# Performance work log

Measured on AMD Instinct MI355X. Metric: run time of the kernel, lower is better.

The kernel has to match this reference:

```python
import jax, jax.numpy as jnp
import numpy as np

B, T, M, E = 2, 2048, 1024, 8
CAP = (2 * B * T) // E  # GShard top-2 capacity = 2*S/E = 1024


def setup_inputs() -> dict:
    key = jax.random.key(0)
    k1, k2, k3 = jax.random.split(key, 3)
    x = jax.random.normal(k1, (B, T, M), jnp.float32)
    wg = jax.random.normal(k2, (M, E), jnp.float32) * 0.02
    expert_w = jax.random.normal(k3, (E, M, M), jnp.float32) * 0.02
    expert_b = jnp.zeros((E, M), jnp.float32)
    return {"x": x, "wg": wg, "expert_w": expert_w, "expert_b": expert_b}


def _top2_gate(x2, wg, capacity):
    """fairseq/GShard Top2Gate (deterministic second-expert, no jitter).
    Returns (l_aux, combine_weights[S,E,C], dispatch_mask[S,E,C] bool)."""
    S = x2.shape[0]
    num_experts = wg.shape[1]
    logits = x2 @ wg                                  # [S, E]
    gates = jax.nn.softmax(logits, axis=-1)           # [S, E]
    # top-1 expert
    idx1 = jnp.argmax(gates, axis=1)
    mask1 = jax.nn.one_hot(idx1, num_experts, dtype=jnp.int32)
    # top-2 expert: argmax over logits with top-1 masked out
    neg_inf = jnp.finfo(logits.dtype).min
    logits_wo1 = jnp.where(mask1.astype(bool), neg_inf, logits)
    idx2 = jnp.argmax(logits_wo1, axis=1)
    mask2 = jax.nn.one_hot(idx2, num_experts, dtype=jnp.int32)
    # positions within each expert's buffer
    loc1 = jnp.cumsum(mask1, axis=0) - 1              # [S, E]
    loc2 = jnp.cumsum(mask2, axis=0) - 1 + jnp.sum(mask1, axis=0, keepdims=True)
    # load-balancing auxiliary loss
    me = jnp.mean(gates, axis=0)
    ce = jnp.mean(mask1.astype(gates.dtype), axis=0)
    l_aux = jnp.mean(me * ce) * (num_experts * num_experts)
    # drop tokens over capacity
    mask1 = mask1 * (loc1 < capacity).astype(jnp.int32)
    mask2 = mask2 * (loc2 < capacity).astype(jnp.int32)
    loc1_s = jnp.sum(loc1 * mask1, axis=1)            # [S]
    loc2_s = jnp.sum(loc2 * mask2, axis=1)
    m1f = mask1.astype(gates.dtype)
    m2f = mask2.astype(gates.dtype)
    gates1_s = jnp.sum(gates * m1f, axis=1)
    gates2_s = jnp.sum(gates * m2f, axis=1)
    denom = gates1_s + gates2_s
    denom = jnp.clip(denom, jnp.finfo(gates.dtype).eps, None)
    gates1 = gates1_s / denom
    gates2 = gates2_s / denom
    loc1_oh = jax.nn.one_hot(loc1_s, capacity, dtype=gates.dtype)  # [S, C]
    loc2_oh = jax.nn.one_hot(loc2_s, capacity, dtype=gates.dtype)
    combine1 = gates1[:, None, None] * m1f[:, :, None] * loc1_oh[:, None, :]
    combine2 = gates2[:, None, None] * m2f[:, :, None] * loc2_oh[:, None, :]
    combine_weights = combine1 + combine2             # [S, E, C]
    dispatch_mask = combine_weights > 0               # bool [S, E, C]
    return l_aux, combine_weights, dispatch_mask


def reference(x, wg, expert_w, expert_b):
    b, t, d = x.shape
    x2 = x.reshape(-1, d)                             # [S, M]
    l_aux, cw, dm = _top2_gate(x2, wg, CAP)
    dmf = dm.astype(x.dtype)                          # [S, E, C]
    # dispatch: (E*C, S) @ (S, M) -> per-expert token buffers [E, C, M]
    dispatched = jnp.einsum('sec,sm->ecm', dmf, x2)
    # per-expert Linear (single device: all experts local, all-to-all = identity)
    expert_out = jnp.einsum('ecm,emn->ecn', dispatched, expert_w) + expert_b[:, None, :]
    # combine: (S, E*C) @ (E*C, M) -> [S, M]
    combined = jnp.einsum('sec,ecm->sm', cw, expert_out)
    return combined.reshape(b, t, d), l_aux
```

## Files before the change

kernel.cpp:

```cpp
#include <hip/hip_runtime.h>

typedef unsigned short u16;
typedef unsigned int u32;
typedef unsigned long long u64;
typedef short v8s __attribute__((ext_vector_type(8)));
typedef float v4f __attribute__((ext_vector_type(4)));

#define S_TOK 4096
#define MDIM  1024
#define NEXP  8
#define CAPN  1024

__device__ __forceinline__ u16 f2bf(float f) {
  u32 u = __float_as_uint(f);
  u += 0x7FFFu + ((u >> 16) & 1u);
  return (u16)(u >> 16);
}
__device__ __forceinline__ float bf2f(u16 h) {
  return __uint_as_float(((u32)h) << 16);
}
__device__ __forceinline__ void gll16(const void* g, void* l) {
  __builtin_amdgcn_global_load_lds(
      (const __attribute__((address_space(1))) void*)g,
      (__attribute__((address_space(3))) void*)l, 16, 0, 0);
}

__global__ __launch_bounds__(256) void prep_kernel(const float* __restrict__ x,
                                                   const float* __restrict__ wg,
                                                   const float* __restrict__ w,
                                                   u16* __restrict__ xbf,
                                                   u16* __restrict__ wT,
                                                   int4* __restrict__ grec,
                                                   float* __restrict__ gpart) {
  __shared__ float smem[8224];
  int tid = threadIdx.x;
  int b = blockIdx.x;
  if (b < 1024) {
    float* wls = smem;
    float (*gsh)[NEXP] = (float (*)[NEXP])(smem + 8192);
    for (int i = tid; i < NEXP * MDIM; i += 256) {
      int m = i >> 3, e = i & 7;
      wls[e * MDIM + m] = wg[i];
    }
    __syncthreads();
    int wave = tid >> 6, lane = tid & 63;
    int s = b * 4 + wave;
    const float* xr = x + (size_t)s * MDIM;
    u16* xw = xbf + (size_t)s * MDIM;
    float acc[NEXP];
#pragma unroll
    for (int e = 0; e < NEXP; e++) acc[e] = 0.f;
#pragma unroll
    for (int j = 0; j < 16; j++) {
      int m = j * 64 + lane;
      float xv = xr[m];
      xw[m] = f2bf(xv);
#pragma unroll
      for (int e = 0; e < NEXP; e++) acc[e] = fmaf(xv, wls[e * MDIM + m], acc[e]);
    }
#pragma unroll
    for (int off = 32; off > 0; off >>= 1)
#pragma unroll
      for (int e = 0; e < NEXP; e++) acc[e] += __shfl_xor(acc[e], off, 64);

    if (lane == 0) {
      float mx = acc[0];
#pragma unroll
      for (int e = 1; e < NEXP; e++) mx = fmaxf(mx, acc[e]);
      float ex[NEXP], sum = 0.f;
#pragma unroll
      for (int e = 0; e < NEXP; e++) { ex[e] = expf(acc[e] - mx); sum += ex[e]; }
      float inv = 1.f / sum;
      int e1 = 0; float b1 = acc[0];
#pragma unroll
      for (int e = 1; e < NEXP; e++) if (acc[e] > b1) { b1 = acc[e]; e1 = e; }
      int e2 = -1; float b2 = -3.4e38f;
#pragma unroll
      for (int e = 0; e < NEXP; e++) if (e != e1 && acc[e] > b2) { b2 = acc[e]; e2 = e; }
      grec[s] = make_int4(e1, e2, __float_as_int(ex[e1] * inv), __float_as_int(ex[e2] * inv));
#pragma unroll
      for (int e = 0; e < NEXP; e++) gsh[wave][e] = ex[e] * inv;
    }
    __syncthreads();
    if (tid < NEXP)
      gpart[b * NEXP + tid] = gsh[0][tid] + gsh[1][tid] + gsh[2][tid] + gsh[3][tid];
  } else {
    int bb = b - 1024;
    int e  = bb >> 8;
    int mt = (bb >> 4) & 15;
    int nt = bb & 15;
    float (*tile)[65] = (float (*)[65])smem;
    const float* src = w + (size_t)e * MDIM * MDIM;
    u16* dst = wT + (size_t)e * MDIM * MDIM;
#pragma unroll
    for (int i = 0; i < 16; i++) {
      int idx = tid + i * 256;
      int r = idx >> 6, c = idx & 63;
      tile[r][c] = src[(size_t)(mt * 64 + r) * MDIM + nt * 64 + c];
    }
    __syncthreads();
#pragma unroll
    for (int i = 0; i < 16; i++) {
      int idx = tid + i * 256;
      int r = idx >> 6, c = idx & 63;
      dst[(size_t)(nt * 64 + r) * MDIM + mt * 64 + c] = f2bf(tile[c][r]);
    }
  }
}

__global__ __launch_bounds__(1024) void scan_kernel(const int4* __restrict__ grec,
                                                    int4* __restrict__ trec,
                                                    int* __restrict__ slot_token,
                                                    const float* __restrict__ gpart,
                                                    u16* __restrict__ zrow,
                                                    float* __restrict__ out) {
  __shared__ u64 wtot[16][4];
  __shared__ float gred[16][NEXP];
  int t = threadIdx.x, lane = t & 63, wave = t >> 6;

#pragma unroll
  for (int i = 0; i < 8; i++) slot_token[t + i * 1024] = -1;
  zrow[t] = 0;

  float4 p0 = ((const float4*)gpart)[t * 2];
  float4 p1 = ((const float4*)gpart)[t * 2 + 1];
  float gs[NEXP] = {p0.x, p0.y, p0.z, p0.w, p1.x, p1.y, p1.z, p1.w};
#pragma unroll
  for (int off = 32; off > 0; off >>= 1)
#pragma unroll
    for (int e = 0; e < NEXP; e++) gs[e] += __shfl_xor(gs[e], off, 64);
  if (lane == 0)
#pragma unroll
    for (int e = 0; e < NEXP; e++) gred[wave][e] = gs[e];

  int4 r[4];
#pragma unroll
  for (int i = 0; i < 4; i++) r[i] = grec[t * 4 + i];

  u64 a1 = 0, b1 = 0, a2 = 0, b2 = 0;
#pragma unroll
  for (int i = 0; i < 4; i++) {
    int x1 = r[i].x, x2 = r[i].y;
    if (x1 < 4) a1 += 1ULL << (x1 * 16); else b1 += 1ULL << ((x1 - 4) * 16);
    if (x2 < 4) a2 += 1ULL << (x2 * 16); else b2 += 1ULL << ((x2 - 4) * 16);
  }
  u64 ia1 = a1, ib1 = b1, ia2 = a2, ib2 = b2;
#pragma unroll
  for (int off = 1; off < 64; off <<= 1) {
    u64 s1 = __shfl_up(a1, off, 64), s2 = __shfl_up(b1, off, 64);
    u64 s3 = __shfl_up(a2, off, 64), s4 = __shfl_up(b2, off, 64);
    if (lane >= off) { a1 += s1; b1 += s2; a2 += s3; b2 += s4; }
  }
  if (lane == 63) { wtot[wave][0] = a1; wtot[wave][1] = b1; wtot[wave][2] = a2; wtot[wave][3] = b2; }
  __syncthreads();
  if (t < 16) {
    u64 v0 = wtot[t][0], v1 = wtot[t][1], v2 = wtot[t][2], v3 = wtot[t][3];
#pragma unroll
    for (int off = 1; off < 16; off <<= 1) {
      u64 s0 = __shfl_up(v0, off, 64), s1 = __shfl_up(v1, off, 64);
      u64 s2 = __shfl_up(v2, off, 64), s3 = __shfl_up(v3, off, 64);
      if (t >= off) { v0 += s0; v1 += s1; v2 += s2; v3 += s3; }
    }
    wtot[t][0] = v0; wtot[t][1] = v1; wtot[t][2] = v2; wtot[t][3] = v3;
  }
  __syncthreads();
  u64 o1 = 0, o2 = 0, o3 = 0, o4 = 0;
  if (wave > 0) { o1 = wtot[wave - 1][0]; o2 = wtot[wave - 1][1]; o3 = wtot[wave - 1][2]; o4 = wtot[wave - 1][3]; }
  u64 ea  = a1 + o1 - ia1;
  u64 eb  = b1 + o2 - ib1;
  u64 ea2 = a2 + o3 - ia2;
  u64 eb2 = b2 + o4 - ib2;
  u64 ta = wtot[15][0], tb = wtot[15][1];

  int base1[NEXP], base2[NEXP], cnt1[NEXP];
#pragma unroll
  for (int e = 0; e < 4; e++) {
    base1[e]     = (int)((ea  >> (e * 16)) & 0xFFFF);
    base1[4 + e] = (int)((eb  >> (e * 16)) & 0xFFFF);
    base2[e]     = (int)((ea2 >> (e * 16)) & 0xFFFF);
    base2[4 + e] = (int)((eb2 >> (e * 16)) & 0xFFFF);
    cnt1[e]      = (int)((ta  >> (e * 16)) & 0xFFFF);
    cnt1[4 + e]  = (int)((tb  >> (e * 16)) & 0xFFFF);
  }
#pragma unroll
  for (int i = 0; i < 4; i++) {
    int s = t * 4 + i;
    int e1 = r[i].x, e2 = r[i].y;
    float g1 = __int_as_float(r[i].z), g2 = __int_as_float(r[i].w);
    int l1 = 0, l2 = 0;
#pragma unroll
    for (int q = 0; q < NEXP; q++) {
      if (q == e1) { l1 = base1[q]; base1[q] = l1 + 1; }
      if (q == e2) { l2 = base2[q]; base2[q] = l2 + 1; }
    }
    int loc2 = l2 + cnt1[e2];
    bool k1 = l1 < CAPN;
    bool k2 = loc2 < CAPN;
    float g1s = k1 ? g1 : 0.f;
    float g2s = k2 ? g2 : 0.f;
    float denom = fmaxf(g1s + g2s, 1.1920929e-7f);
    float gn1 = g1s / denom, gn2 = g2s / denom;
    int slot1 = k1 ? e1 * CAPN + l1 : -1;
    int slot2 = k2 ? e2 * CAPN + loc2 : -1;
    trec[s] = make_int4(slot1, slot2, __float_as_int(gn1), __float_as_int(gn2));
    if (k1) slot_token[slot1] = s;
    if (k2) slot_token[slot2] = s;
  }
  if (t == 0) {
    float acc = 0.f;
#pragma unroll
    for (int e = 0; e < NEXP; e++) {
      float g = 0.f;
      for (int w2 = 0; w2 < 16; w2++) g += gred[w2][e];
      acc += g * (float)cnt1[e];
    }
    out[(size_t)S_TOK * MDIM] = 8.f * acc / (4096.f * 4096.f);
  }
}

__global__ __launch_bounds__(256, 2) void expert_gemm(const u16* __restrict__ xbf,
                                                      const u16* __restrict__ wT,
                                                      const int* __restrict__ slot_token,
                                                      const u16* __restrict__ zrow,
                                                      const float* __restrict__ bias,
                                                      u16* __restrict__ eoutb) {
  __shared__ __align__(16) u16 As[128 * 64];
  __shared__ __align__(16) u16 Bs[128 * 64];
  const int tid  = threadIdx.x;
  const int e    = blockIdx.x >> 6;
  const int tile = blockIdx.x & 63;
  const int tm   = (tile >> 3) << 7;
  const int tn   = (tile & 7) << 7;
  const int lane = tid & 63;
  const int wave = tid >> 6;
  const int wr = wave >> 1, wc = wave & 1;

  const u16* srcA[4];
  const u16* srcB[4];
#pragma unroll
  for (int it = 0; it < 4; ++it) {
    int g     = it * 4 + wave;
    int m_loc = (g >> 1) * 16 + (lane & 15);
    int kc    = (g & 1) * 4 + (lane >> 4);
    int st    = slot_token[e * CAPN + tm + m_loc];
    srcA[it] = (st >= 0 ? xbf + (size_t)st * MDIM : zrow) + kc * 8;
    srcB[it] = wT + (size_t)e * MDIM * MDIM + (size_t)(tn + m_loc) * MDIM + kc * 8;
  }
  char* ldsA = (char*)As;
  char* ldsB = (char*)Bs;

  v4f acc[4][4];
#pragma unroll
  for (int i = 0; i < 4; i++)
#pragma unroll
    for (int j = 0; j < 4; j++) acc[i][j] = (v4f){0.f, 0.f, 0.f, 0.f};

  for (int k0 = 0; k0 < MDIM; k0 += 64) {
    __syncthreads();
#pragma unroll
    for (int it = 0; it < 4; ++it)
      gll16(srcA[it] + k0, ldsA + tid * 16 + it * 4096);
#pragma unroll
    for (int it = 0; it < 4; ++it)
      gll16(srcB[it] + k0, ldsB + tid * 16 + it * 4096);
    __syncthreads();

    const v8s* Ap = (const v8s*)As;
    const v8s* Bp = (const v8s*)Bs;
#pragma unroll
    for (int ks = 0; ks < 2; ++ks) {
      v8s af[4], bfr[4];
#pragma unroll
      for (int i = 0; i < 4; i++)
        af[i] = Ap[((wr * 4 + i) * 2 + ks) * 64 + lane];
#pragma unroll
      for (int j = 0; j < 4; j++)
        bfr[j] = Bp[((wc * 4 + j) * 2 + ks) * 64 + lane];
#pragma unroll
      for (int i = 0; i < 4; i++)
#pragma unroll
        for (int j = 0; j < 4; j++)
          acc[i][j] = __builtin_amdgcn_mfma_f32_16x16x32_bf16(af[i], bfr[j], acc[i][j], 0, 0, 0);
    }
  }

  const float* bp = bias + (size_t)e * MDIM;
  float bv[4];
#pragma unroll
  for (int j = 0; j < 4; j++) bv[j] = bp[tn + wc * 64 + j * 16 + (lane & 15)];
  u16* outp = eoutb + (size_t)e * CAPN * MDIM;
#pragma unroll
  for (int i = 0; i < 4; i++) {
#pragma unroll
    for (int rr = 0; rr < 4; rr++) {
      int row = tm + wr * 64 + i * 16 + (lane >> 4) * 4 + rr;
#pragma unroll
      for (int j = 0; j < 4; j++) {
        int col = tn + wc * 64 + j * 16 + (lane & 15);
        outp[(size_t)row * MDIM + col] = f2bf(acc[i][j][rr] + bv[j]);
      }
    }
  }
}

__global__ __launch_bounds__(256) void combine_kernel(const u16* __restrict__ eoutb,
                                                      const int4* __restrict__ trec,
                                                      float* __restrict__ out) {
  int s = blockIdx.x;
  int tid = threadIdx.x;
  int4 r = trec[s];
  float g1 = __int_as_float(r.z), g2 = __int_as_float(r.w);
  float4 res = make_float4(0.f, 0.f, 0.f, 0.f);
  if (r.x >= 0) {
    ushort4 o = ((const ushort4*)(eoutb + (size_t)r.x * MDIM))[tid];
    res.x += g1 * bf2f(o.x); res.y += g1 * bf2f(o.y);
    res.z += g1 * bf2f(o.z); res.w += g1 * bf2f(o.w);
  }
  if (r.y >= 0) {
    ushort4 o = ((const ushort4*)(eoutb + (size_t)r.y * MDIM))[tid];
    res.x += g2 * bf2f(o.x); res.y += g2 * bf2f(o.y);
    res.z += g2 * bf2f(o.z); res.w += g2 * bf2f(o.w);
  }
  ((float4*)out)[(size_t)s * 256 + tid] = res;
}

extern "C" void kernel_launch(void* const* d_in, const int* in_sizes, int n_in,
                              void* d_out, int out_size, void* d_ws, size_t ws_size,
                              hipStream_t stream) {
  (void)in_sizes; (void)n_in; (void)out_size; (void)ws_size;
  const float* x  = (const float*)d_in[0];
  const float* wg = (const float*)d_in[1];
  const float* ew = (const float*)d_in[2];
  const float* eb = (const float*)d_in[3];
  float* out = (float*)d_out;

  char* ws = (char*)d_ws;
  u16*   xbf   = (u16*)(ws + 0);
  u16*   wT    = (u16*)(ws + 8388608);
  u16*   eoutb = (u16*)(ws + 25165824);
  u16*   zrow  = (u16*)(ws + 41943040);
  int4*  grec  = (int4*)(ws + 41945088);
  int4*  trec  = (int4*)(ws + 42010624);
  int*   slot  = (int*)(ws + 42076160);
  float* gpart = (float*)(ws + 42108928);

  prep_kernel<<<3072, 256, 0, stream>>>(x, wg, ew, xbf, wT, grec, gpart);
  scan_kernel<<<1, 1024, 0, stream>>>(grec, trec, slot, gpart, zrow, out);
  expert_gemm<<<512, 256, 0, stream>>>(xbf, wT, slot, zrow, eb, eoutb);
  combine_kernel<<<4096, 256, 0, stream>>>(eoutb, trec, out);
}
```

Before: 150.6 us.

## Split expert GEMM along K into two partial outputs, reduce in combine

The expert GEMM is split along K into two halves, which doubles the grid from 512 to 1024 blocks so all CUs get enough work. Each half writes its own bf16 partial buffer. The combine kernel sums the two partials, adds the bias, and applies the gate weights. The LDS load layout also changes to row-major chunks, with matching fragment indexing. This adds extra write and read traffic for the second partial buffer and rounds each partial to bf16 before the sum, which adds some precision loss.

```diff
diff --git a/kernel.cpp b/kernel.cpp
--- a/kernel.cpp
+++ b/kernel.cpp
@@ -10,6 +10,7 @@
 #define MDIM  1024
 #define NEXP  8
 #define CAPN  1024
+#define PART_ELEMS (NEXP * CAPN * MDIM)
 
 __device__ __forceinline__ u16 f2bf(float f) {
   u32 u = __float_as_uint(f);
@@ -222,13 +223,14 @@
                                                       const u16* __restrict__ wT,
                                                       const int* __restrict__ slot_token,
                                                       const u16* __restrict__ zrow,
-                                                      const float* __restrict__ bias,
                                                       u16* __restrict__ eoutb) {
   __shared__ __align__(16) u16 As[128 * 64];
   __shared__ __align__(16) u16 Bs[128 * 64];
   const int tid  = threadIdx.x;
-  const int e    = blockIdx.x >> 6;
-  const int tile = blockIdx.x & 63;
+  const int bx   = blockIdx.x;
+  const int kh   = bx >> 9;
+  const int e    = (bx >> 6) & 7;
+  const int tile = bx & 63;
   const int tm   = (tile >> 3) << 7;
   const int tn   = (tile & 7) << 7;
   const int lane = tid & 63;
@@ -239,12 +241,12 @@
   const u16* srcB[4];
 #pragma unroll
   for (int it = 0; it < 4; ++it) {
-    int g     = it * 4 + wave;
-    int m_loc = (g >> 1) * 16 + (lane & 15);
-    int kc    = (g & 1) * 4 + (lane >> 4);
-    int st    = slot_token[e * CAPN + tm + m_loc];
-    srcA[it] = (st >= 0 ? xbf + (size_t)st * MDIM : zrow) + kc * 8;
-    srcB[it] = wT + (size_t)e * MDIM * MDIM + (size_t)(tn + m_loc) * MDIM + kc * 8;
+    int off = tid * 16 + it * 4096;
+    int row = off >> 7;
+    int kb  = off & 127;
+    int st  = slot_token[e * CAPN + tm + row];
+    srcA[it] = (st >= 0 ? xbf + (size_t)st * MDIM : zrow) + (kb >> 1);
+    srcB[it] = wT + (size_t)e * MDIM * MDIM + (size_t)(tn + row) * MDIM + (kb >> 1);
   }
   char* ldsA = (char*)As;
   char* ldsB = (char*)Bs;
@@ -255,7 +257,8 @@
 #pragma unroll
     for (int j = 0; j < 4; j++) acc[i][j] = (v4f){0.f, 0.f, 0.f, 0.f};
 
-  for (int k0 = 0; k0 < MDIM; k0 += 64) {
+  const int kbeg = kh * 512;
+  for (int k0 = kbeg; k0 < kbeg + 512; k0 += 64) {
     __syncthreads();
 #pragma unroll
     for (int it = 0; it < 4; ++it)
@@ -272,10 +275,10 @@
       v8s af[4], bfr[4];
 #pragma unroll
       for (int i = 0; i < 4; i++)
-        af[i] = Ap[((wr * 4 + i) * 2 + ks) * 64 + lane];
+        af[i] = Ap[(wr * 64 + i * 16 + (lane & 15)) * 8 + ks * 4 + (lane >> 4)];
 #pragma unroll
       for (int j = 0; j < 4; j++)
-        bfr[j] = Bp[((wc * 4 + j) * 2 + ks) * 64 + lane];
+        bfr[j] = Bp[(wc * 64 + j * 16 + (lane & 15)) * 8 + ks * 4 + (lane >> 4)];
 #pragma unroll
       for (int i = 0; i < 4; i++)
 #pragma unroll
@@ -284,11 +287,7 @@
     }
   }
 
-  const float* bp = bias + (size_t)e * MDIM;
-  float bv[4];
-#pragma unroll
-  for (int j = 0; j < 4; j++) bv[j] = bp[tn + wc * 64 + j * 16 + (lane & 15)];
-  u16* outp = eoutb + (size_t)e * CAPN * MDIM;
+  u16* outp = eoutb + (size_t)kh * PART_ELEMS + (size_t)e * CAPN * MDIM;
 #pragma unroll
   for (int i = 0; i < 4; i++) {
 #pragma unroll
@@ -297,7 +296,7 @@
 #pragma unroll
       for (int j = 0; j < 4; j++) {
         int col = tn + wc * 64 + j * 16 + (lane & 15);
-        outp[(size_t)row * MDIM + col] = f2bf(acc[i][j][rr] + bv[j]);
+        outp[(size_t)row * MDIM + col] = f2bf(acc[i][j][rr]);
       }
     }
   }
@@ -305,21 +304,33 @@
 
 __global__ __launch_bounds__(256) void combine_kernel(const u16* __restrict__ eoutb,
                                                       const int4* __restrict__ trec,
+                                                      const float* __restrict__ bias,
                                                       float* __restrict__ out) {
   int s = blockIdx.x;
   int tid = threadIdx.x;
   int4 r = trec[s];
   float g1 = __int_as_float(r.z), g2 = __int_as_float(r.w);
   float4 res = make_float4(0.f, 0.f, 0.f, 0.f);
+  const ushort4* p0 = (const ushort4*)eoutb;
+  const ushort4* p1 = (const ushort4*)(eoutb + (size_t)PART_ELEMS);
+  const float4*  b4 = (const float4*)bias;
   if (r.x >= 0) {
-    ushort4 o = ((const ushort4*)(eoutb + (size_t)r.x * MDIM))[tid];
-    res.x += g1 * bf2f(o.x); res.y += g1 * bf2f(o.y);
-    res.z += g1 * bf2f(o.z); res.w += g1 * bf2f(o.w);
+    ushort4 a = p0[(size_t)r.x * 256 + tid];
+    ushort4 b = p1[(size_t)r.x * 256 + tid];
+    float4  c = b4[(size_t)(r.x >> 10) * 256 + tid];
+    res.x += g1 * (bf2f(a.x) + bf2f(b.x) + c.x);
+    res.y += g1 * (bf2f(a.y) + bf2f(b.y) + c.y);
+    res.z += g1 * (bf2f(a.z) + bf2f(b.z) + c.z);
+    res.w += g1 * (bf2f(a.w) + bf2f(b.w) + c.w);
   }
   if (r.y >= 0) {
-    ushort4 o = ((const ushort4*)(eoutb + (size_t)r.y * MDIM))[tid];
-    res.x += g2 * bf2f(o.x); res.y += g2 * bf2f(o.y);
-    res.z += g2 * bf2f(o.z); res.w += g2 * bf2f(o.w);
+    ushort4 a = p0[(size_t)r.y * 256 + tid];
+    ushort4 b = p1[(size_t)r.y * 256 + tid];
+    float4  c = b4[(size_t)(r.y >> 10) * 256 + tid];
+    res.x += g2 * (bf2f(a.x) + bf2f(b.x) + c.x);
+    res.y += g2 * (bf2f(a.y) + bf2f(b.y) + c.y);
+    res.z += g2 * (bf2f(a.z) + bf2f(b.z) + c.z);
+    res.w += g2 * (bf2f(a.w) + bf2f(b.w) + c.w);
   }
   ((float4*)out)[(size_t)s * 256 + tid] = res;
 }
@@ -338,14 +349,14 @@
   u16*   xbf   = (u16*)(ws + 0);
   u16*   wT    = (u16*)(ws + 8388608);
   u16*   eoutb = (u16*)(ws + 25165824);
-  u16*   zrow  = (u16*)(ws + 41943040);
-  int4*  grec  = (int4*)(ws + 41945088);
-  int4*  trec  = (int4*)(ws + 42010624);
-  int*   slot  = (int*)(ws + 42076160);
-  float* gpart = (float*)(ws + 42108928);
+  u16*   zrow  = (u16*)(ws + 58720256);
+  int4*  grec  = (int4*)(ws + 58722304);
+  int4*  trec  = (int4*)(ws + 58787840);
+  int*   slot  = (int*)(ws + 58853376);
+  float* gpart = (float*)(ws + 58886144);
 
   prep_kernel<<<3072, 256, 0, stream>>>(x, wg, ew, xbf, wT, grec, gpart);
   scan_kernel<<<1, 1024, 0, stream>>>(grec, trec, slot, gpart, zrow, out);
-  expert_gemm<<<512, 256, 0, stream>>>(xbf, wT, slot, zrow, eb, eoutb);
-  combine_kernel<<<4096, 256, 0, stream>>>(eoutb, trec, out);
-}
+  expert_gemm<<<1024, 256, 0, stream>>>(xbf, wT, slot, zrow, eoutb);
+  combine_kernel<<<4096, 256, 0, stream>>>(eoutb, trec, eb, out);
+}
```

Result: faster. 142.4 us (-5.4%).
